# Kernel tuning notes

Hardware: AMD Instinct MI355X
Metric: run time of the kernel (lower is better)

Reference implementation:

```python
import jax, jax.numpy as jnp
import numpy as np

OUT, IN, B = 11008, 4096, 32

def setup_inputs() -> dict:
    key = jax.random.key(0)
    k1, k2, k3, k4 = jax.random.split(key, 4)
    x = jax.random.normal(k1, (B, IN), dtype=jnp.float32)
    # ternary weights in {-1, 0, +1}, stored as int (int8 semantics)
    weight_q = jax.random.randint(k2, (OUT, IN), -1, 2, dtype=jnp.int32)
    # per-row positive scale (fp16 in torch, cast to fp32 at dequant time)
    weight_scale = jax.random.uniform(k3, (OUT, 1), dtype=jnp.float32, minval=0.01, maxval=1.0)
    bias = jax.random.normal(k4, (OUT,), dtype=jnp.float32)
    return {"x": x, "weight_q": weight_q, "weight_scale": weight_scale, "bias": bias}

def reference(x, weight_q, weight_scale, bias):
    # dequantize_2bit: int8 ternary * per-row scale -> fp32 weight [OUT, IN]
    W = weight_q.astype(jnp.float32) * weight_scale.astype(jnp.float32)
    # F.linear: x @ W.T + bias
    return jnp.einsum('bi,oi->bo', x.astype(jnp.float32), W) + bias
```

## Files before the change

kernel.cpp:

```cpp
#include <hip/hip_runtime.h>

#define OUT_N 11008
#define IN_K  4096
#define BATCH 32
#define SEGS  16
#define KSEG  (IN_K / SEGS)
#define OPB   64
#define XSTR  264
#define TOT   (BATCH * OUT_N)

typedef __attribute__((ext_vector_type(8))) short short8;
typedef __attribute__((ext_vector_type(4))) float float4v;
typedef __attribute__((ext_vector_type(4))) int int4v;

__device__ __forceinline__ unsigned short f2bf(float f) {
    unsigned u = __builtin_bit_cast(unsigned, f);
    unsigned r = u + 0x7FFFu + ((u >> 16) & 1u);
    return (unsigned short)(r >> 16);
}

__device__ __forceinline__ unsigned pkbf16(float fhi, float flo) {
    return __builtin_amdgcn_perm(__builtin_bit_cast(unsigned, fhi),
                                 __builtin_bit_cast(unsigned, flo),
                                 0x07060302u);
}

__global__ __launch_bounds__(256, 8) void lin2bit_kernel(
    const int* __restrict__ wq, const float* __restrict__ scale,
    const float* __restrict__ x, float* __restrict__ ws)
{
    __shared__ unsigned short xs[BATCH][XSTR];

    const int t    = threadIdx.x;
    const int lane = t & 63;
    const int wave = t >> 6;
    const int kseg = blockIdx.y * KSEG;
    const int o0   = blockIdx.x * OPB;

#pragma unroll
    for (int it = 0; it < 8; ++it) {
        int idx = it * 256 + t;
        int b   = idx >> 6;
        int k4  = idx & 63;
        float4 v = *reinterpret_cast<const float4*>(x + b * IN_K + kseg + k4 * 4);
        ushort4 h = { f2bf(v.x), f2bf(v.y), f2bf(v.z), f2bf(v.w) };
        *reinterpret_cast<ushort4*>(&xs[b][k4 * 4]) = h;
    }
    __syncthreads();

    const int quad = lane >> 4;
    const int l16  = lane & 15;
    const int o    = o0 + wave * 16 + l16;

    const int* __restrict__ wp = wq + (size_t)o * IN_K + kseg + quad * 8;
    const unsigned short* x0 = &xs[l16][quad * 8];
    const unsigned short* x1 = &xs[l16 + 16][quad * 8];

    float4v acc0 = {0.f, 0.f, 0.f, 0.f};
    float4v acc1 = {0.f, 0.f, 0.f, 0.f};

#pragma unroll
    for (int ki = 0; ki < KSEG; ki += 32) {
        int4v w0 = __builtin_nontemporal_load(reinterpret_cast<const int4v*>(wp + ki));
        int4v w1 = __builtin_nontemporal_load(reinterpret_cast<const int4v*>(wp + ki + 4));
        uint4 bw;
        bw.x = pkbf16((float)w0.y, (float)w0.x);
        bw.y = pkbf16((float)w0.w, (float)w0.z);
        bw.z = pkbf16((float)w1.y, (float)w1.x);
        bw.w = pkbf16((float)w1.w, (float)w1.z);
        short8 bf = __builtin_bit_cast(short8, bw);
        short8 a0 = *reinterpret_cast<const short8*>(x0 + ki);
        short8 a1 = *reinterpret_cast<const short8*>(x1 + ki);
        acc0 = __builtin_amdgcn_mfma_f32_16x16x32_bf16(a0, bf, acc0, 0, 0, 0);
        acc1 = __builtin_amdgcn_mfma_f32_16x16x32_bf16(a1, bf, acc1, 0, 0, 0);
    }

    const float s = scale[o];
    const int b0 = quad * 4;
    float* __restrict__ wsp = ws + (size_t)blockIdx.y * TOT + o;
#pragma unroll
    for (int r = 0; r < 4; ++r) {
        wsp[(size_t)(b0 + r)      * OUT_N] = s * acc0[r];
        wsp[(size_t)(b0 + r + 16) * OUT_N] = s * acc1[r];
    }
}

__global__ __launch_bounds__(256) void reduce_kernel(
    const float* __restrict__ ws, const float* __restrict__ bias,
    float* __restrict__ out)
{
    int i4 = (blockIdx.x * 256 + threadIdx.x) * 4;
    int o  = i4 % OUT_N;
    float4v acc = *reinterpret_cast<const float4v*>(bias + o);
#pragma unroll
    for (int sgi = 0; sgi < SEGS; ++sgi) {
        float4v p = *reinterpret_cast<const float4v*>(ws + (size_t)sgi * TOT + i4);
        acc += p;
    }
    *reinterpret_cast<float4v*>(out + i4) = acc;
}

extern "C" void kernel_launch(void* const* d_in, const int* in_sizes, int n_in,
                              void* d_out, int out_size, void* d_ws, size_t ws_size,
                              hipStream_t stream) {
    const float* x     = (const float*)d_in[0];
    const int*   wq    = (const int*)d_in[1];
    const float* scale = (const float*)d_in[2];
    const float* bias  = (const float*)d_in[3];
    float* out = (float*)d_out;
    float* ws  = (float*)d_ws;

    lin2bit_kernel<<<dim3(OUT_N / OPB, SEGS), 256, 0, stream>>>(wq, scale, x, ws);
    reduce_kernel<<<dim3(TOT / 1024), 256, 0, stream>>>(ws, bias, out);
}
```

Measured before the change: 259.6 us.

## Stream weight tiles into LDS via async global_load_lds double buffering

Weight loads now go straight from global memory into a per-wave double-buffered LDS region using global_load_lds, with an XOR swizzle so the MFMA operand reads avoid bank conflicts. Two stages are prefetched ahead and vmcnt waits control consumption, so loads overlap with conversion and MFMA work. LDS use grows and the occupancy hint drops from 8 to 4 blocks per CU. The hand-written vmcnt waits also count the x staging loads, which adds some ordering risk.

```diff
diff --git a/kernel.cpp b/kernel.cpp
--- a/kernel.cpp
+++ b/kernel.cpp
@@ -1,10 +1,12 @@
 #include <hip/hip_runtime.h>
+#include <stdint.h>
 
 #define OUT_N 11008
 #define IN_K  4096
 #define BATCH 32
 #define SEGS  16
 #define KSEG  (IN_K / SEGS)
+#define NSTEP (KSEG / 32)
 #define OPB   64
 #define XSTR  264
 #define TOT   (BATCH * OUT_N)
@@ -25,17 +27,39 @@
                                  0x07060302u);
 }
 
-__global__ __launch_bounds__(256, 8) void lin2bit_kernel(
+typedef const __attribute__((address_space(1))) int* gas_t;
+typedef __attribute__((address_space(3))) int* las_t;
+__device__ __forceinline__ void gll16(const int* g, int* l) {
+    __builtin_amdgcn_global_load_lds((gas_t)g, (las_t)l, 16, 0, 2);
+}
+
+__global__ __launch_bounds__(256, 4) void lin2bit_kernel(
     const int* __restrict__ wq, const float* __restrict__ scale,
     const float* __restrict__ x, float* __restrict__ ws)
 {
     __shared__ unsigned short xs[BATCH][XSTR];
+    __shared__ int wlds[4][2][512];
 
     const int t    = threadIdx.x;
     const int lane = t & 63;
     const int wave = t >> 6;
     const int kseg = blockIdx.y * KSEG;
     const int o0   = blockIdx.x * OPB;
+
+    const int srow = lane >> 3;
+    const int slot = lane & 7;
+    const int chnk = slot ^ srow;
+    const int* g0 = wq + (size_t)(o0 + wave * 16 + srow)     * IN_K + kseg + chnk * 4;
+    const int* g1 = wq + (size_t)(o0 + wave * 16 + srow + 8) * IN_K + kseg + chnk * 4;
+    int* lb0 = &wlds[wave][0][0];
+    int* lb1 = &wlds[wave][1][0];
+
+#define STAGE(s) do { int* _lb = ((s) & 1) ? lb1 : lb0; \
+        gll16(g0 + (s) * 32, _lb); \
+        gll16(g1 + (s) * 32, _lb + 256); } while (0)
+
+    STAGE(0);
+    STAGE(1);
 
 #pragma unroll
     for (int it = 0; it < 8; ++it) {
@@ -52,36 +76,42 @@
     const int l16  = lane & 15;
     const int o    = o0 + wave * 16 + l16;
 
-    const int* __restrict__ wp = wq + (size_t)o * IN_K + kseg + quad * 8;
     const unsigned short* x0 = &xs[l16][quad * 8];
     const unsigned short* x1 = &xs[l16 + 16][quad * 8];
+    const int off0 = l16 * 32 + (((2 * quad)     ^ (l16 & 7)) * 4);
+    const int off1 = l16 * 32 + (((2 * quad + 1) ^ (l16 & 7)) * 4);
 
     float4v acc0 = {0.f, 0.f, 0.f, 0.f};
     float4v acc1 = {0.f, 0.f, 0.f, 0.f};
 
 #pragma unroll
-    for (int ki = 0; ki < KSEG; ki += 32) {
-        int4v w0 = __builtin_nontemporal_load(reinterpret_cast<const int4v*>(wp + ki));
-        int4v w1 = __builtin_nontemporal_load(reinterpret_cast<const int4v*>(wp + ki + 4));
+    for (int s = 0; s < NSTEP; ++s) {
+        if (s == NSTEP - 1) { asm volatile("s_waitcnt vmcnt(0)" ::: "memory"); }
+        else                { asm volatile("s_waitcnt vmcnt(2)" ::: "memory"); }
+        const int* wb = (s & 1) ? lb1 : lb0;
+        int4v w0 = *reinterpret_cast<const int4v*>(wb + off0);
+        int4v w1 = *reinterpret_cast<const int4v*>(wb + off1);
+        short8 a0 = *reinterpret_cast<const short8*>(x0 + s * 32);
+        short8 a1 = *reinterpret_cast<const short8*>(x1 + s * 32);
+        if (s < NSTEP - 2) STAGE(s + 2);
         uint4 bw;
         bw.x = pkbf16((float)w0.y, (float)w0.x);
         bw.y = pkbf16((float)w0.w, (float)w0.z);
         bw.z = pkbf16((float)w1.y, (float)w1.x);
         bw.w = pkbf16((float)w1.w, (float)w1.z);
         short8 bf = __builtin_bit_cast(short8, bw);
-        short8 a0 = *reinterpret_cast<const short8*>(x0 + ki);
-        short8 a1 = *reinterpret_cast<const short8*>(x1 + ki);
         acc0 = __builtin_amdgcn_mfma_f32_16x16x32_bf16(a0, bf, acc0, 0, 0, 0);
         acc1 = __builtin_amdgcn_mfma_f32_16x16x32_bf16(a1, bf, acc1, 0, 0, 0);
     }
+#undef STAGE
 
-    const float s = scale[o];
+    const float sc = scale[o];
     const int b0 = quad * 4;
     float* __restrict__ wsp = ws + (size_t)blockIdx.y * TOT + o;
 #pragma unroll
     for (int r = 0; r < 4; ++r) {
-        wsp[(size_t)(b0 + r)      * OUT_N] = s * acc0[r];
-        wsp[(size_t)(b0 + r + 16) * OUT_N] = s * acc1[r];
+        wsp[(size_t)(b0 + r)      * OUT_N] = sc * acc0[r];
+        wsp[(size_t)(b0 + r + 16) * OUT_N] = sc * acc1[r];
     }
 }
 
```

After: 254.6 us. No clear change (-1.9%).
